# Optimization experiments

Hardware: AMD Instinct MI355X
Metric: run time of the kernel (lower is better)

The kernel has to match this reference:

```python
import math
import jax, jax.numpy as jnp
import numpy as np

B, T, DIM, H = 2, 2048, 2048, 16
D = DIM // H  # head_dim = 128


def setup_inputs() -> dict:
    key = jax.random.key(0)
    ks = jax.random.split(key, 6)
    s = 0.02
    x = jax.random.normal(ks[0], (B, T, DIM), dtype=jnp.float32)
    # causal mask: True = keep, False = masked (matches masked_fill(mask==0, -inf))
    attn_mask = jnp.tril(jnp.ones((T, T), dtype=bool))[None, None, :, :]
    Wq = jax.random.normal(ks[1], (DIM, DIM), dtype=jnp.float32) * s
    Wk = jax.random.normal(ks[2], (DIM, D), dtype=jnp.float32) * s
    Wv = jax.random.normal(ks[3], (DIM, D), dtype=jnp.float32) * s
    Wo = jax.random.normal(ks[4], (DIM, DIM), dtype=jnp.float32) * s
    return {
        "x": x, "attn_mask": attn_mask,
        "Wq": Wq, "bq": jnp.zeros((DIM,), jnp.float32),
        "Wk": Wk, "bk": jnp.zeros((D,), jnp.float32),
        "Wv": Wv, "bv": jnp.zeros((D,), jnp.float32),
        "Wo": Wo, "bo": jnp.zeros((DIM,), jnp.float32),
    }


def _rope_freqs(t_len, d):
    inv_freq = 1.0 / (10000.0 ** (jnp.arange(0, d, 2, dtype=jnp.float32) / d))
    f = jnp.arange(t_len, dtype=jnp.float32)[:, None] * inv_freq[None, :]  # [T, d/2]
    # duplicate to full head dim so cos/sin align with rotate_half's half split
    cos = jnp.concatenate([jnp.cos(f), jnp.cos(f)], axis=-1)[None, None]  # [1,1,T,d]
    sin = jnp.concatenate([jnp.sin(f), jnp.sin(f)], axis=-1)[None, None]
    return cos, sin


def _rotate_half(u):
    d2 = u.shape[-1] // 2
    return jnp.concatenate([-u[..., d2:], u[..., :d2]], axis=-1)


def reference(x, attn_mask, Wq, bq, Wk, bk, Wv, bv, Wo, bo):
    Bx, Tx, C = x.shape
    q = (x @ Wq + bq).reshape(Bx, Tx, H, D).transpose(0, 2, 1, 3)  # [B,H,T,D]
    k = (x @ Wk + bk)[:, None]  # [B,1,T,D] single shared KV head (MQA)
    v = (x @ Wv + bv)[:, None]
    cos, sin = _rope_freqs(Tx, D)
    q = q * cos + _rotate_half(q) * sin
    k = k * cos + _rotate_half(k) * sin
    attn = jnp.matmul(q, k.swapaxes(-2, -1)) / math.sqrt(D)  # [B,H,T,T]
    attn = jnp.where(attn_mask, attn, jnp.float32(-jnp.inf))
    attn = jax.nn.softmax(attn, axis=-1)
    out = jnp.matmul(attn, v)  # [B,H,T,D]
    out = out.transpose(0, 2, 1, 3).reshape(Bx, Tx, C)
    return out @ Wo + bo
```

## Files before the change

kernel.cpp:

```cpp
#include <hip/hip_runtime.h>

typedef unsigned short u16;
typedef unsigned int u32;
typedef __bf16 bf16x8 __attribute__((ext_vector_type(8)));
typedef float f32x4 __attribute__((ext_vector_type(4)));
typedef float f32x16 __attribute__((ext_vector_type(16)));
typedef u32 u32x4 __attribute__((ext_vector_type(4)));

__device__ __forceinline__ u16 bfu(float x) {
  union { __bf16 h; u16 u; } z; z.h = (__bf16)x; return z.u;
}
__device__ __forceinline__ u32 pk2(float a, float b) {
  union { __bf16 h[2]; u32 u; } z;
  z.h[0] = (__bf16)a; z.h[1] = (__bf16)b;
  return z.u;
}
__device__ __forceinline__ void gl_lds16(const u16* g, u16* l) {
  __builtin_amdgcn_global_load_lds((const __attribute__((address_space(1))) void*)g,
                                   (__attribute__((address_space(3))) void*)l, 16, 0, 0);
}

__global__ __launch_bounds__(256) void cvt_bf16(const float* __restrict__ src, u16* __restrict__ dst, int n8) {
  int i = blockIdx.x * 256 + threadIdx.x;
  if (i >= n8) return;
  const float4* s4 = (const float4*)src;
  float4 a = s4[2 * i], b = s4[2 * i + 1];
  u32x4 o;
  o[0] = pk2(a.x, a.y); o[1] = pk2(a.z, a.w);
  o[2] = pk2(b.x, b.y); o[3] = pk2(b.z, b.w);
  ((u32x4*)dst)[i] = o;
}

__global__ void transpose_cvt(const float* __restrict__ src, u16* __restrict__ dst, int R, int C) {
  __shared__ float tile[32][33];
  const int c0 = blockIdx.x * 32, r0 = blockIdx.y * 32;
  const int tx = threadIdx.x, ty = threadIdx.y;
#pragma unroll
  for (int i = 0; i < 4; ++i)
    tile[ty + i * 8][tx] = src[(size_t)(r0 + ty + i * 8) * C + c0 + tx];
  __syncthreads();
#pragma unroll
  for (int i = 0; i < 4; ++i)
    dst[(size_t)(c0 + ty + i * 8) * R + r0 + tx] = bfu(tile[tx][ty + i * 8]);
}

__global__ void transpose_v(const float* __restrict__ QKV, const float* __restrict__ bv, u16* __restrict__ Vt) {
  __shared__ float tile[32][33];
  const int t0 = blockIdx.x * 32, d0 = blockIdx.y * 32, b = blockIdx.z;
  const int tx = threadIdx.x, ty = threadIdx.y;
#pragma unroll
  for (int i = 0; i < 4; ++i)
    tile[ty + i * 8][tx] = QKV[(size_t)(b * 2048 + t0 + ty + i * 8) * 2304 + 2176 + d0 + tx] + bv[d0 + tx];
  __syncthreads();
#pragma unroll
  for (int i = 0; i < 4; ++i)
    Vt[(size_t)b * 262144 + (size_t)(d0 + ty + i * 8) * 2048 + t0 + tx] = bfu(tile[tx][ty + i * 8]);
}

__global__ __launch_bounds__(256) void rope_qk(const float* __restrict__ QKV, const float* __restrict__ bq,
                                               const float* __restrict__ bk,
                                               u16* __restrict__ Qb, u16* __restrict__ Kb) {
  const int row = blockIdx.x;
  const int b = row >> 11, t = row & 2047;
  const int tid = threadIdx.x;
  const float* qrow = QKV + (size_t)row * 2304;
  const float scale = 0.1275173862437171f;
  const float nl2 = -0.20762050593046f;
#pragma unroll
  for (int it = 0; it < 4; ++it) {
    int idx = tid + it * 256;
    int h = idx >> 6, j = idx & 63;
    float q0 = qrow[h * 128 + j] + bq[h * 128 + j];
    float q1 = qrow[h * 128 + j + 64] + bq[h * 128 + j + 64];
    float ang = (float)t * exp2f((float)j * nl2);
    float s, c;
    __sincosf(ang, &s, &c);
    size_t o = ((size_t)((b * 16 + h) * 2048 + t)) * 128 + j;
    Qb[o]      = bfu((q0 * c - q1 * s) * scale);
    Qb[o + 64] = bfu((q1 * c + q0 * s) * scale);
  }
  if (tid < 64) {
    int j = tid;
    float k0 = qrow[2048 + j] + bk[j];
    float k1 = qrow[2048 + j + 64] + bk[j + 64];
    float ang = (float)t * exp2f((float)j * nl2);
    float s, c;
    __sincosf(ang, &s, &c);
    size_t o = (size_t)row * 128 + j;
    Kb[o]      = bfu(k0 * c - k1 * s);
    Kb[o + 64] = bfu(k1 * c + k0 * s);
  }
}

template <bool BIAS, int NTL>
__global__ __launch_bounds__(256) void gemm_bt(const u16* __restrict__ A, const u16* __restrict__ Bt,
                                               const float* __restrict__ bias, float* __restrict__ C,
                                               int M, int N, int K) {
  const int lin = blockIdx.x;
  const int xcd = lin & 7, idx = lin >> 3;
  constexpr int HALF = NTL / 2;
  const int ly = idx / HALF, lx = idx - ly * HALF;
  const int my = (xcd >> 1) * 8 + ly;
  const int nx = (xcd & 1) * HALF + lx;
  const int n0 = nx * 128, m0 = my * 128;
  const int tid = threadIdx.x, lane = tid & 63;
  const int wid = tid >> 6, wr = wid >> 1, wc = wid & 1;
  __shared__ __align__(16) u16 As[128 * 32];
  __shared__ __align__(16) u16 Bs[128 * 32];
  f32x4 acc[4][4];
#pragma unroll
  for (int i = 0; i < 4; ++i)
#pragma unroll
    for (int j = 0; j < 4; ++j)
#pragma unroll
      for (int rr = 0; rr < 4; ++rr) acc[i][j][rr] = 0.f;

  const int c0 = tid, c1 = tid + 256;
  const int ar0 = c0 >> 2, ac0 = (c0 & 3) * 8;
  const int ar1 = c1 >> 2, ac1 = (c1 & 3) * 8;
  const int r = lane & 15, g = lane >> 4;

  for (int k0 = 0; k0 < K; k0 += 32) {
    gl_lds16(A + (size_t)(m0 + ar0) * K + k0 + ac0, As + c0 * 8);
    gl_lds16(A + (size_t)(m0 + ar1) * K + k0 + ac1, As + c1 * 8);
    gl_lds16(Bt + (size_t)(n0 + ar0) * K + k0 + ac0, Bs + c0 * 8);
    gl_lds16(Bt + (size_t)(n0 + ar1) * K + k0 + ac1, Bs + c1 * 8);
    __syncthreads();
    bf16x8 af[4], bfr[4];
#pragma unroll
    for (int mi = 0; mi < 4; ++mi)
      af[mi] = *reinterpret_cast<const bf16x8*>(&As[(wr * 64 + mi * 16 + r) * 32 + g * 8]);
#pragma unroll
    for (int ni = 0; ni < 4; ++ni)
      bfr[ni] = *reinterpret_cast<const bf16x8*>(&Bs[(wc * 64 + ni * 16 + r) * 32 + g * 8]);
#pragma unroll
    for (int mi = 0; mi < 4; ++mi)
#pragma unroll
      for (int ni = 0; ni < 4; ++ni)
        acc[mi][ni] = __builtin_amdgcn_mfma_f32_16x16x32_bf16(af[mi], bfr[ni], acc[mi][ni], 0, 0, 0);
    __syncthreads();
  }
#pragma unroll
  for (int mi = 0; mi < 4; ++mi)
#pragma unroll
    for (int ni = 0; ni < 4; ++ni) {
      int col = n0 + wc * 64 + ni * 16 + r;
      float bia = BIAS ? bias[col] : 0.f;
#pragma unroll
      for (int reg = 0; reg < 4; ++reg) {
        int row = m0 + wr * 64 + mi * 16 + g * 4 + reg;
        C[(size_t)row * N + col] = acc[mi][ni][reg] + bia;
      }
    }
}

__global__ __launch_bounds__(256, 2) void attn_kernel(const u16* __restrict__ Qb, const u16* __restrict__ Kb,
                                                      const u16* __restrict__ Vt, u16* __restrict__ Ob) {
  const int bid = blockIdx.x;
  const int grp = bid >> 5;
  const int chunk = (bid < 256) ? (15 - grp) : (grp - 8);
  const int bh = bid & 31, h = bh & 15, b = bh >> 4;
  const int tid = threadIdx.x, wid = tid >> 6, lane = tid & 63;
  const int l31 = lane & 31, hf = lane >> 5;

  __shared__ __align__(16) u16 smem[32768];
  u16* Ksb = smem;
  u16* Vsb = smem + 16384;

  const u16* Kbase = Kb + (size_t)b * 2048 * 128;
  const u16* Vbase = Vt + (size_t)b * 128 * 2048;

  int krow[4], kcol[4], vrow[4], vcol[4];
#pragma unroll
  for (int i = 0; i < 4; ++i) {
    const int seg = wid * 4 + i;
    const int r = seg * 4 + (lane >> 4);
    krow[i] = r; kcol[i] = (((lane & 15) ^ (r & 15)) << 3);
    const int d = seg * 8 + (lane >> 3);
    vrow[i] = d; vcol[i] = (((lane & 7) ^ (d & 7)) << 3);
  }
  const int ldsoff = wid * 2048 + lane * 8;

#define STAGE(buf, kvb_) do {                                                              \
    _Pragma("unroll") for (int i_ = 0; i_ < 4; ++i_)                                       \
      gl_lds16(Kbase + (size_t)((kvb_) + krow[i_]) * 128 + kcol[i_],                       \
               &Ksb[(buf) * 8192 + ldsoff + i_ * 512]);                                    \
    _Pragma("unroll") for (int i_ = 0; i_ < 4; ++i_)                                       \
      gl_lds16(Vbase + (size_t)vrow[i_] * 2048 + (kvb_) + vcol[i_],                        \
               &Vsb[(buf) * 8192 + ldsoff + i_ * 512]);                                    \
  } while (0)

  const int xk16 = l31 & 15;
  const int xk8 = l31 & 7;

  const int cb = chunk * 128;
  const int qw = cb + wid * 32;
  const u16* qptr = Qb + ((size_t)((b * 16 + h) * 2048 + qw + l31)) * 128;
  bf16x8 qf[8];
#pragma unroll
  for (int c = 0; c < 8; ++c)
    qf[c] = *reinterpret_cast<const bf16x8*>(qptr + c * 16 + hf * 8);

  f32x16 ot[4];
#pragma unroll
  for (int dt = 0; dt < 4; ++dt)
#pragma unroll
    for (int rr = 0; rr < 16; ++rr) ot[dt][rr] = 0.f;
  float m = -1e30f, lsum = 0.f;

  const int nkv = 2 * chunk + 2;
  STAGE(0, 0);
  for (int it = 0; it < nkv; ++it) {
    const int kvb = it << 6, cur = it & 1;
    if (it + 1 < nkv) {
      STAGE(cur ^ 1, kvb + 64);
      asm volatile("s_waitcnt vmcnt(8)" ::: "memory");
    } else {
      asm volatile("s_waitcnt vmcnt(0)" ::: "memory");
    }
    __builtin_amdgcn_s_barrier();

    if (kvb <= qw) {
      const u16* ks = Ksb + cur * 8192;
      const u16* vs = Vsb + cur * 8192;
      f32x16 st0, st1;
#pragma unroll
      for (int rr = 0; rr < 16; ++rr) { st0[rr] = 0.f; st1[rr] = -1e30f; }
      const u16* ksr0 = ks + l31 * 128;
#pragma unroll
      for (int c = 0; c < 8; ++c) {
        bf16x8 kf = *reinterpret_cast<const bf16x8*>(ksr0 + (((2 * c + hf) ^ xk16) << 3));
        st0 = __builtin_amdgcn_mfma_f32_32x32x16_bf16(kf, qf[c], st0, 0, 0, 0);
      }
      const bool a1 = (kvb + 32 <= qw);
      if (a1) {
#pragma unroll
        for (int rr = 0; rr < 16; ++rr) st1[rr] = 0.f;
        const u16* ksr1 = ks + (32 + l31) * 128;
#pragma unroll
        for (int c = 0; c < 8; ++c) {
          bf16x8 kf = *reinterpret_cast<const bf16x8*>(ksr1 + (((2 * c + hf) ^ xk16) << 3));
          st1 = __builtin_amdgcn_mfma_f32_32x32x16_bf16(kf, qf[c], st1, 0, 0, 0);
        }
        if (kvb + 32 == qw) {
#pragma unroll
          for (int rr = 0; rr < 16; ++rr) {
            int kvl = (rr & 3) + 8 * (rr >> 2) + 4 * hf;
            if (kvl > l31) st1[rr] = -1e30f;
          }
        }
      }
      if (kvb == qw) {
#pragma unroll
        for (int rr = 0; rr < 16; ++rr) {
          int kvl = (rr & 3) + 8 * (rr >> 2) + 4 * hf;
          if (kvl > l31) st0[rr] = -1e30f;
        }
      }

      float tmax = st0[0];
#pragma unroll
      for (int rr = 1; rr < 16; ++rr) tmax = fmaxf(tmax, st0[rr]);
#pragma unroll
      for (int rr = 0; rr < 16; ++rr) tmax = fmaxf(tmax, st1[rr]);
      tmax = fmaxf(tmax, __shfl_xor(tmax, 32, 64));
      if (!__all(tmax - m <= 8.f)) {
        const float mnew = fmaxf(m, tmax);
        const float alpha = exp2f(m - mnew);
        lsum *= alpha;
#pragma unroll
        for (int dt = 0; dt < 4; ++dt)
#pragma unroll
          for (int rr = 0; rr < 16; ++rr) ot[dt][rr] *= alpha;
        m = mnew;
      }
      float rsum = 0.f;
#pragma unroll
      for (int rr = 0; rr < 16; ++rr) { st0[rr] = exp2f(st0[rr] - m); rsum += st0[rr]; }
#pragma unroll
      for (int rr = 0; rr < 16; ++rr) { st1[rr] = exp2f(st1[rr] - m); rsum += st1[rr]; }
      rsum += __shfl_xor(rsum, 32, 64);
      lsum += rsum;

#pragma unroll
      for (int n = 0; n < 2; ++n) {
        if (n == 1 && !a1) break;
        const f32x16& pp = n ? st1 : st0;
#pragma unroll
        for (int s = 0; s < 2; ++s) {
          u32 a0p = pk2(pp[8 * s + 0], pp[8 * s + 1]);
          u32 a1p = pk2(pp[8 * s + 2], pp[8 * s + 3]);
          u32 b0p = pk2(pp[8 * s + 4], pp[8 * s + 5]);
          u32 b1p = pk2(pp[8 * s + 6], pp[8 * s + 7]);
          u32 k0 = hf ? b0p : a0p, k1 = hf ? b1p : a1p;
          u32 sd0 = hf ? a0p : b0p, sd1 = hf ? a1p : b1p;
          u32 r0 = (u32)__shfl_xor((int)sd0, 32, 64);
          u32 r1 = (u32)__shfl_xor((int)sd1, 32, 64);
          u32x4 pw;
          pw[0] = hf ? r0 : k0; pw[1] = hf ? r1 : k1;
          pw[2] = hf ? k0 : r0; pw[3] = hf ? k1 : r1;
          bf16x8 pb = __builtin_bit_cast(bf16x8, pw);
          const int cc = n * 4 + s * 2 + hf;
#pragma unroll
          for (int dt = 0; dt < 4; ++dt) {
            bf16x8 vf = *reinterpret_cast<const bf16x8*>(
                &vs[(dt * 32 + l31) * 64 + ((cc ^ xk8) << 3)]);
            ot[dt] = __builtin_amdgcn_mfma_f32_32x32x16_bf16(vf, pb, ot[dt], 0, 0, 0);
          }
        }
      }
    }
    __builtin_amdgcn_s_barrier();
  }

  u16* myt = smem + wid * (32 * 136);
  const float inv = 1.f / lsum;
#pragma unroll
  for (int dt = 0; dt < 4; ++dt)
#pragma unroll
    for (int rq = 0; rq < 4; ++rq) {
      int d = dt * 32 + 8 * rq + 4 * hf;
      u32 lo = pk2(ot[dt][rq * 4 + 0] * inv, ot[dt][rq * 4 + 1] * inv);
      u32 hi = pk2(ot[dt][rq * 4 + 2] * inv, ot[dt][rq * 4 + 3] * inv);
      u32* dstp = (u32*)&myt[l31 * 136 + d];
      dstp[0] = lo; dstp[1] = hi;
    }
  __syncthreads();
  const size_t outbase = ((size_t)(b * 2048 + qw)) * 2048 + h * 128;
#pragma unroll
  for (int i = 0; i < 8; ++i) {
    int chunk2 = i * 64 + lane;
    int row = chunk2 >> 4, c16 = chunk2 & 15;
    u32x4 v = *reinterpret_cast<const u32x4*>(&myt[row * 136 + c16 * 8]);
    *reinterpret_cast<u32x4*>(Ob + outbase + (size_t)row * 2048 + c16 * 8) = v;
  }
#undef STAGE
}

extern "C" void kernel_launch(void* const* d_in, const int* in_sizes, int n_in,
                              void* d_out, int out_size, void* d_ws, size_t ws_size,
                              hipStream_t stream) {
  const float* x  = (const float*)d_in[0];
  const float* Wq = (const float*)d_in[2];
  const float* bq = (const float*)d_in[3];
  const float* Wk = (const float*)d_in[4];
  const float* bk = (const float*)d_in[5];
  const float* Wv = (const float*)d_in[6];
  const float* bv = (const float*)d_in[7];
  const float* Wo = (const float*)d_in[8];
  const float* bo = (const float*)d_in[9];

  char* ws = (char*)d_ws;
  u16*  xb    = (u16*)ws;   ws += (size_t)4096 * 2048 * 2;
  u16*  WqkvT = (u16*)ws;   ws += (size_t)2304 * 2048 * 2;
  u16*  WoT   = (u16*)ws;   ws += (size_t)2048 * 2048 * 2;
  float* QKV  = (float*)ws; ws += (size_t)4096 * 2304 * 4;
  u16*  Qb    = (u16*)ws;   ws += (size_t)2 * 16 * 2048 * 128 * 2;
  u16*  Kb    = (u16*)ws;   ws += (size_t)2 * 2048 * 128 * 2;
  u16*  Vt    = (u16*)ws;   ws += (size_t)2 * 128 * 2048 * 2;
  u16*  Ob    = (u16*)ws;   ws += (size_t)4096 * 2048 * 2;

  dim3 tb(32, 8);
  cvt_bf16<<<4096, 256, 0, stream>>>(x, xb, 1048576);
  transpose_cvt<<<dim3(64, 64), tb, 0, stream>>>(Wq, WqkvT, 2048, 2048);
  transpose_cvt<<<dim3(4, 64),  tb, 0, stream>>>(Wk, WqkvT + (size_t)2048 * 2048, 2048, 128);
  transpose_cvt<<<dim3(4, 64),  tb, 0, stream>>>(Wv, WqkvT + (size_t)2176 * 2048, 2048, 128);
  transpose_cvt<<<dim3(64, 64), tb, 0, stream>>>(Wo, WoT, 2048, 2048);

  gemm_bt<false, 18><<<576, 256, 0, stream>>>(xb, WqkvT, nullptr, QKV, 4096, 2304, 2048);
  rope_qk<<<4096, 256, 0, stream>>>(QKV, bq, bk, Qb, Kb);
  transpose_v<<<dim3(64, 4, 2), tb, 0, stream>>>(QKV, bv, Vt);
  attn_kernel<<<512, 256, 0, stream>>>(Qb, Kb, Vt, Ob);
  gemm_bt<true, 16><<<512, 256, 0, stream>>>(Ob, WoT, bo, (float*)d_out, 4096, 2048, 2048);
}
```

Before: 223.9 us.

## Split long causal query chunks across two KV partitions with a combine kernel

The eight longest query chunks (c=8..15) are split into two blocks, each covering half of the KV range, which raises the attention grid from 512 to 768 blocks and evens out per-block work. Partial outputs in fp32 plus the running max and sum are written to workspace, and a new combine kernel merges them with a log-sum-exp rescale and writes bf16. This targets load imbalance and tail effects from the causal triangle. The cost is an extra kernel launch and extra fp32 global traffic.

New measurement: 240.4 us. +7.3%, slower.

```diff
diff --git a/kernel.cpp b/kernel.cpp
--- a/kernel.cpp
+++ b/kernel.cpp
@@ -155,11 +155,17 @@
 }
 
 __global__ __launch_bounds__(256, 2) void attn_kernel(const u16* __restrict__ Qb, const u16* __restrict__ Kb,
-                                                      const u16* __restrict__ Vt, u16* __restrict__ Ob) {
-  const int bid = blockIdx.x;
-  const int grp = bid >> 5;
-  const int chunk = (bid < 256) ? (15 - grp) : (grp - 8);
-  const int bh = bid & 31, h = bh & 15, b = bh >> 4;
+                                                      const u16* __restrict__ Vt, u16* __restrict__ Ob,
+                                                      float* __restrict__ Opart, float2* __restrict__ Ostat) {
+  const int pid = blockIdx.x;
+  const int local = pid >> 5, bh = pid & 31;
+  const int h = bh & 15, b = bh >> 4;
+  int c, part, npart;
+  if (local < 16) { c = 15 - (local >> 1); part = local & 1; npart = 2; }
+  else            { c = 23 - local;        part = 0;         npart = 1; }
+  const int tlo = part * (c + 1);
+  const int thi = (npart == 2 && part == 0) ? (c + 1) : (2 * c + 2);
+
   const int tid = threadIdx.x, wid = tid >> 6, lane = tid & 63;
   const int l31 = lane & 31, hf = lane >> 5;
 
@@ -193,13 +199,12 @@
   const int xk16 = l31 & 15;
   const int xk8 = l31 & 7;
 
-  const int cb = chunk * 128;
-  const int qw = cb + wid * 32;
+  const int qw = c * 128 + wid * 32;
   const u16* qptr = Qb + ((size_t)((b * 16 + h) * 2048 + qw + l31)) * 128;
   bf16x8 qf[8];
 #pragma unroll
-  for (int c = 0; c < 8; ++c)
-    qf[c] = *reinterpret_cast<const bf16x8*>(qptr + c * 16 + hf * 8);
+  for (int cc2 = 0; cc2 < 8; ++cc2)
+    qf[cc2] = *reinterpret_cast<const bf16x8*>(qptr + cc2 * 16 + hf * 8);
 
   f32x16 ot[4];
 #pragma unroll
@@ -208,11 +213,10 @@
     for (int rr = 0; rr < 16; ++rr) ot[dt][rr] = 0.f;
   float m = -1e30f, lsum = 0.f;
 
-  const int nkv = 2 * chunk + 2;
-  STAGE(0, 0);
-  for (int it = 0; it < nkv; ++it) {
-    const int kvb = it << 6, cur = it & 1;
-    if (it + 1 < nkv) {
+  STAGE(0, tlo * 64);
+  for (int it = tlo; it < thi; ++it) {
+    const int kvb = it << 6, cur = (it - tlo) & 1;
+    if (it + 1 < thi) {
       STAGE(cur ^ 1, kvb + 64);
       asm volatile("s_waitcnt vmcnt(8)" ::: "memory");
     } else {
@@ -228,9 +232,9 @@
       for (int rr = 0; rr < 16; ++rr) { st0[rr] = 0.f; st1[rr] = -1e30f; }
       const u16* ksr0 = ks + l31 * 128;
 #pragma unroll
-      for (int c = 0; c < 8; ++c) {
-        bf16x8 kf = *reinterpret_cast<const bf16x8*>(ksr0 + (((2 * c + hf) ^ xk16) << 3));
-        st0 = __builtin_amdgcn_mfma_f32_32x32x16_bf16(kf, qf[c], st0, 0, 0, 0);
+      for (int cc2 = 0; cc2 < 8; ++cc2) {
+        bf16x8 kf = *reinterpret_cast<const bf16x8*>(ksr0 + (((2 * cc2 + hf) ^ xk16) << 3));
+        st0 = __builtin_amdgcn_mfma_f32_32x32x16_bf16(kf, qf[cc2], st0, 0, 0, 0);
       }
       const bool a1 = (kvb + 32 <= qw);
       if (a1) {
@@ -238,9 +242,9 @@
         for (int rr = 0; rr < 16; ++rr) st1[rr] = 0.f;
         const u16* ksr1 = ks + (32 + l31) * 128;
 #pragma unroll
-        for (int c = 0; c < 8; ++c) {
-          bf16x8 kf = *reinterpret_cast<const bf16x8*>(ksr1 + (((2 * c + hf) ^ xk16) << 3));
-          st1 = __builtin_amdgcn_mfma_f32_32x32x16_bf16(kf, qf[c], st1, 0, 0, 0);
+        for (int cc2 = 0; cc2 < 8; ++cc2) {
+          bf16x8 kf = *reinterpret_cast<const bf16x8*>(ksr1 + (((2 * cc2 + hf) ^ xk16) << 3));
+          st1 = __builtin_amdgcn_mfma_f32_32x32x16_bf16(kf, qf[cc2], st1, 0, 0, 0);
         }
         if (kvb + 32 == qw) {
 #pragma unroll
@@ -313,28 +317,78 @@
     __builtin_amdgcn_s_barrier();
   }
 
-  u16* myt = smem + wid * (32 * 136);
-  const float inv = 1.f / lsum;
-#pragma unroll
-  for (int dt = 0; dt < 4; ++dt)
-#pragma unroll
-    for (int rq = 0; rq < 4; ++rq) {
-      int d = dt * 32 + 8 * rq + 4 * hf;
-      u32 lo = pk2(ot[dt][rq * 4 + 0] * inv, ot[dt][rq * 4 + 1] * inv);
-      u32 hi = pk2(ot[dt][rq * 4 + 2] * inv, ot[dt][rq * 4 + 3] * inv);
-      u32* dstp = (u32*)&myt[l31 * 136 + d];
-      dstp[0] = lo; dstp[1] = hi;
+  if (npart == 1) {
+    u16* myt = smem + wid * (32 * 136);
+    const float inv = 1.f / lsum;
+#pragma unroll
+    for (int dt = 0; dt < 4; ++dt)
+#pragma unroll
+      for (int rq = 0; rq < 4; ++rq) {
+        int d = dt * 32 + 8 * rq + 4 * hf;
+        u32 lo = pk2(ot[dt][rq * 4 + 0] * inv, ot[dt][rq * 4 + 1] * inv);
+        u32 hi = pk2(ot[dt][rq * 4 + 2] * inv, ot[dt][rq * 4 + 3] * inv);
+        u32* dstp = (u32*)&myt[l31 * 136 + d];
+        dstp[0] = lo; dstp[1] = hi;
+      }
+    __syncthreads();
+    const size_t outbase = ((size_t)(b * 2048 + qw)) * 2048 + h * 128;
+#pragma unroll
+    for (int i = 0; i < 8; ++i) {
+      int chunk2 = i * 64 + lane;
+      int row = chunk2 >> 4, c16 = chunk2 & 15;
+      u32x4 v = *reinterpret_cast<const u32x4*>(&myt[row * 136 + c16 * 8]);
+      *reinterpret_cast<u32x4*>(Ob + outbase + (size_t)row * 2048 + c16 * 8) = v;
     }
-  __syncthreads();
-  const size_t outbase = ((size_t)(b * 2048 + qw)) * 2048 + h * 128;
+  } else {
+    const int pslot = (((c - 8) << 5) + bh) * 2 + part;
+    if (hf == 0) {
+      float2 st; st.x = m; st.y = lsum;
+      Ostat[pslot * 128 + wid * 32 + l31] = st;
+    }
+    float* Op = Opart + (size_t)pslot * 16384 + (size_t)(wid * 32 + l31) * 128;
+#pragma unroll
+    for (int dt = 0; dt < 4; ++dt)
+#pragma unroll
+      for (int rq = 0; rq < 4; ++rq) {
+        f32x4 v;
+        v[0] = ot[dt][rq * 4 + 0]; v[1] = ot[dt][rq * 4 + 1];
+        v[2] = ot[dt][rq * 4 + 2]; v[3] = ot[dt][rq * 4 + 3];
+        *reinterpret_cast<f32x4*>(Op + dt * 32 + 8 * rq + 4 * hf) = v;
+      }
+  }
+#undef STAGE
+}
+
+__global__ __launch_bounds__(256) void attn_combine(const float* __restrict__ Opart,
+                                                    const float2* __restrict__ Ostat,
+                                                    u16* __restrict__ Ob) {
+  const int gid = blockIdx.x;
+  const int cm = gid >> 5, bh = gid & 31;
+  const int c = cm + 8, h = bh & 15, b = bh >> 4;
+  const int tid = threadIdx.x;
+  const int row = tid >> 1, half = tid & 1;
+  const int p0 = gid * 2, p1 = p0 + 1;
+  const float2 s0 = Ostat[p0 * 128 + row];
+  const float2 s1 = Ostat[p1 * 128 + row];
+  const float M = fmaxf(s0.x, s1.x);
+  float a0 = exp2f(s0.x - M), a1 = exp2f(s1.x - M);
+  const float inv = 1.f / (a0 * s0.y + a1 * s1.y);
+  a0 *= inv; a1 *= inv;
+  const f32x4* O0 = (const f32x4*)(Opart + (size_t)p0 * 16384 + row * 128 + half * 64);
+  const f32x4* O1 = (const f32x4*)(Opart + (size_t)p1 * 16384 + row * 128 + half * 64);
+  u32 w[32];
+#pragma unroll
+  for (int i = 0; i < 16; ++i) {
+    f32x4 v0 = O0[i], v1 = O1[i];
+    w[i * 2]     = pk2(a0 * v0[0] + a1 * v1[0], a0 * v0[1] + a1 * v1[1]);
+    w[i * 2 + 1] = pk2(a0 * v0[2] + a1 * v1[2], a0 * v0[3] + a1 * v1[3]);
+  }
+  u16* dst = Ob + ((size_t)(b * 2048 + c * 128 + row)) * 2048 + h * 128 + half * 64;
 #pragma unroll
   for (int i = 0; i < 8; ++i) {
-    int chunk2 = i * 64 + lane;
-    int row = chunk2 >> 4, c16 = chunk2 & 15;
-    u32x4 v = *reinterpret_cast<const u32x4*>(&myt[row * 136 + c16 * 8]);
-    *reinterpret_cast<u32x4*>(Ob + outbase + (size_t)row * 2048 + c16 * 8) = v;
-  }
-#undef STAGE
+    u32x4 v; v[0] = w[i * 4]; v[1] = w[i * 4 + 1]; v[2] = w[i * 4 + 2]; v[3] = w[i * 4 + 3];
+    ((u32x4*)dst)[i] = v;
+  }
 }
 
 extern "C" void kernel_launch(void* const* d_in, const int* in_sizes, int n_in,
@@ -359,6 +413,8 @@
   u16*  Kb    = (u16*)ws;   ws += (size_t)2 * 2048 * 128 * 2;
   u16*  Vt    = (u16*)ws;   ws += (size_t)2 * 128 * 2048 * 2;
   u16*  Ob    = (u16*)ws;   ws += (size_t)4096 * 2048 * 2;
+  float* Opart = (float*)ws; ws += (size_t)512 * 128 * 128 * 4;
+  float2* Ostat = (float2*)ws; ws += (size_t)512 * 128 * 8;
 
   dim3 tb(32, 8);
   cvt_bf16<<<4096, 256, 0, stream>>>(x, xb, 1048576);
@@ -370,6 +426,7 @@
   gemm_bt<false, 18><<<576, 256, 0, stream>>>(xb, WqkvT, nullptr, QKV, 4096, 2304, 2048);
   rope_qk<<<4096, 256, 0, stream>>>(QKV, bq, bk, Qb, Kb);
   transpose_v<<<dim3(64, 4, 2), tb, 0, stream>>>(QKV, bv, Vt);
-  attn_kernel<<<512, 256, 0, stream>>>(Qb, Kb, Vt, Ob);
+  attn_kernel<<<768, 256, 0, stream>>>(Qb, Kb, Vt, Ob, Opart, Ostat);
+  attn_combine<<<256, 256, 0, stream>>>(Opart, Ostat, Ob);
   gemm_bt<true, 16><<<512, 256, 0, stream>>>(Ob, WoT, bo, (float*)d_out, 4096, 2048, 2048);
 }
```

## Split attention into 64-row, 2-wave blocks with single-buffered KV and MFMA priority

Applied to the files above, without the earlier changes.

Attention blocks shrink from 4 waves covering 128 query rows to 2 waves covering 64 rows. The grid doubles to 1024 blocks, ordered longest-chunk first, which should give finer causal load balance and let more blocks share a CU. KV staging changes from double-buffered prefetch to a single buffer that is loaded and then synchronised, halving LDS per block but exposing load latency inside each iteration. s_setprio raises wave priority around the MFMA sections, and the per-wave causal skip of whole tiles is dropped because every wave now needs each staged tile.

Measured after the change: 236.9 us. 1.06x slower.

```diff
diff --git a/kernel.cpp b/kernel.cpp
--- a/kernel.cpp
+++ b/kernel.cpp
@@ -154,47 +154,45 @@
     }
 }
 
-__global__ __launch_bounds__(256, 2) void attn_kernel(const u16* __restrict__ Qb, const u16* __restrict__ Kb,
+__global__ __launch_bounds__(128, 2) void attn_kernel(const u16* __restrict__ Qb, const u16* __restrict__ Kb,
                                                       const u16* __restrict__ Vt, u16* __restrict__ Ob) {
   const int bid = blockIdx.x;
-  const int grp = bid >> 5;
-  const int chunk = (bid < 256) ? (15 - grp) : (grp - 8);
+  const int chunk = 31 - (bid >> 5);
   const int bh = bid & 31, h = bh & 15, b = bh >> 4;
   const int tid = threadIdx.x, wid = tid >> 6, lane = tid & 63;
   const int l31 = lane & 31, hf = lane >> 5;
 
-  __shared__ __align__(16) u16 smem[32768];
-  u16* Ksb = smem;
-  u16* Vsb = smem + 16384;
+  __shared__ __align__(16) u16 smem[16384];
+  u16* Ks = smem;
+  u16* Vs = smem + 8192;
 
   const u16* Kbase = Kb + (size_t)b * 2048 * 128;
   const u16* Vbase = Vt + (size_t)b * 128 * 2048;
 
-  int krow[4], kcol[4], vrow[4], vcol[4];
-#pragma unroll
-  for (int i = 0; i < 4; ++i) {
-    const int seg = wid * 4 + i;
+  int krow[8], kcol[8], vrow[8], vcol[8];
+#pragma unroll
+  for (int i = 0; i < 8; ++i) {
+    const int seg = wid * 8 + i;
     const int r = seg * 4 + (lane >> 4);
     krow[i] = r; kcol[i] = (((lane & 15) ^ (r & 15)) << 3);
     const int d = seg * 8 + (lane >> 3);
     vrow[i] = d; vcol[i] = (((lane & 7) ^ (d & 7)) << 3);
   }
-  const int ldsoff = wid * 2048 + lane * 8;
-
-#define STAGE(buf, kvb_) do {                                                              \
-    _Pragma("unroll") for (int i_ = 0; i_ < 4; ++i_)                                       \
+  const int ldsoff = wid * 4096 + lane * 8;
+
+#define STAGE(kvb_) do {                                                                   \
+    _Pragma("unroll") for (int i_ = 0; i_ < 8; ++i_)                                       \
       gl_lds16(Kbase + (size_t)((kvb_) + krow[i_]) * 128 + kcol[i_],                       \
-               &Ksb[(buf) * 8192 + ldsoff + i_ * 512]);                                    \
-    _Pragma("unroll") for (int i_ = 0; i_ < 4; ++i_)                                       \
+               &Ks[ldsoff + i_ * 512]);                                                    \
+    _Pragma("unroll") for (int i_ = 0; i_ < 8; ++i_)                                       \
       gl_lds16(Vbase + (size_t)vrow[i_] * 2048 + (kvb_) + vcol[i_],                        \
-               &Vsb[(buf) * 8192 + ldsoff + i_ * 512]);                                    \
+               &Vs[ldsoff + i_ * 512]);                                                    \
   } while (0)
 
   const int xk16 = l31 & 15;
   const int xk8 = l31 & 7;
 
-  const int cb = chunk * 128;
-  const int qw = cb + wid * 32;
+  const int qw = chunk * 64 + wid * 32;
   const u16* qptr = Qb + ((size_t)((b * 16 + h) * 2048 + qw + l31)) * 128;
   bf16x8 qf[8];
 #pragma unroll
@@ -208,109 +206,105 @@
     for (int rr = 0; rr < 16; ++rr) ot[dt][rr] = 0.f;
   float m = -1e30f, lsum = 0.f;
 
-  const int nkv = 2 * chunk + 2;
-  STAGE(0, 0);
+  const int nkv = chunk + 1;
   for (int it = 0; it < nkv; ++it) {
-    const int kvb = it << 6, cur = it & 1;
-    if (it + 1 < nkv) {
-      STAGE(cur ^ 1, kvb + 64);
-      asm volatile("s_waitcnt vmcnt(8)" ::: "memory");
-    } else {
-      asm volatile("s_waitcnt vmcnt(0)" ::: "memory");
-    }
-    __builtin_amdgcn_s_barrier();
-
-    if (kvb <= qw) {
-      const u16* ks = Ksb + cur * 8192;
-      const u16* vs = Vsb + cur * 8192;
-      f32x16 st0, st1;
-#pragma unroll
-      for (int rr = 0; rr < 16; ++rr) { st0[rr] = 0.f; st1[rr] = -1e30f; }
-      const u16* ksr0 = ks + l31 * 128;
+    const int kvb = it << 6;
+    STAGE(kvb);
+    __syncthreads();
+
+    f32x16 st0, st1;
+#pragma unroll
+    for (int rr = 0; rr < 16; ++rr) { st0[rr] = 0.f; st1[rr] = -1e30f; }
+    const u16* ksr0 = Ks + l31 * 128;
+    __builtin_amdgcn_s_setprio(1);
+#pragma unroll
+    for (int c = 0; c < 8; ++c) {
+      bf16x8 kf = *reinterpret_cast<const bf16x8*>(ksr0 + (((2 * c + hf) ^ xk16) << 3));
+      st0 = __builtin_amdgcn_mfma_f32_32x32x16_bf16(kf, qf[c], st0, 0, 0, 0);
+    }
+    __builtin_amdgcn_s_setprio(0);
+    const bool a1 = (kvb + 32 <= qw);
+    if (a1) {
+#pragma unroll
+      for (int rr = 0; rr < 16; ++rr) st1[rr] = 0.f;
+      const u16* ksr1 = Ks + (32 + l31) * 128;
+      __builtin_amdgcn_s_setprio(1);
 #pragma unroll
       for (int c = 0; c < 8; ++c) {
-        bf16x8 kf = *reinterpret_cast<const bf16x8*>(ksr0 + (((2 * c + hf) ^ xk16) << 3));
-        st0 = __builtin_amdgcn_mfma_f32_32x32x16_bf16(kf, qf[c], st0, 0, 0, 0);
-      }
-      const bool a1 = (kvb + 32 <= qw);
-      if (a1) {
-#pragma unroll
-        for (int rr = 0; rr < 16; ++rr) st1[rr] = 0.f;
-        const u16* ksr1 = ks + (32 + l31) * 128;
-#pragma unroll
-        for (int c = 0; c < 8; ++c) {
-          bf16x8 kf = *reinterpret_cast<const bf16x8*>(ksr1 + (((2 * c + hf) ^ xk16) << 3));
-          st1 = __builtin_amdgcn_mfma_f32_32x32x16_bf16(kf, qf[c], st1, 0, 0, 0);
-        }
-        if (kvb + 32 == qw) {
-#pragma unroll
-          for (int rr = 0; rr < 16; ++rr) {
-            int kvl = (rr & 3) + 8 * (rr >> 2) + 4 * hf;
-            if (kvl > l31) st1[rr] = -1e30f;
-          }
-        }
-      }
-      if (kvb == qw) {
+        bf16x8 kf = *reinterpret_cast<const bf16x8*>(ksr1 + (((2 * c + hf) ^ xk16) << 3));
+        st1 = __builtin_amdgcn_mfma_f32_32x32x16_bf16(kf, qf[c], st1, 0, 0, 0);
+      }
+      __builtin_amdgcn_s_setprio(0);
+      if (kvb + 32 == qw) {
 #pragma unroll
         for (int rr = 0; rr < 16; ++rr) {
           int kvl = (rr & 3) + 8 * (rr >> 2) + 4 * hf;
-          if (kvl > l31) st0[rr] = -1e30f;
+          if (kvl > l31) st1[rr] = -1e30f;
         }
       }
-
-      float tmax = st0[0];
-#pragma unroll
-      for (int rr = 1; rr < 16; ++rr) tmax = fmaxf(tmax, st0[rr]);
-#pragma unroll
-      for (int rr = 0; rr < 16; ++rr) tmax = fmaxf(tmax, st1[rr]);
-      tmax = fmaxf(tmax, __shfl_xor(tmax, 32, 64));
-      if (!__all(tmax - m <= 8.f)) {
-        const float mnew = fmaxf(m, tmax);
-        const float alpha = exp2f(m - mnew);
-        lsum *= alpha;
-#pragma unroll
-        for (int dt = 0; dt < 4; ++dt)
-#pragma unroll
-          for (int rr = 0; rr < 16; ++rr) ot[dt][rr] *= alpha;
-        m = mnew;
-      }
-      float rsum = 0.f;
-#pragma unroll
-      for (int rr = 0; rr < 16; ++rr) { st0[rr] = exp2f(st0[rr] - m); rsum += st0[rr]; }
-#pragma unroll
-      for (int rr = 0; rr < 16; ++rr) { st1[rr] = exp2f(st1[rr] - m); rsum += st1[rr]; }
-      rsum += __shfl_xor(rsum, 32, 64);
-      lsum += rsum;
-
-#pragma unroll
-      for (int n = 0; n < 2; ++n) {
-        if (n == 1 && !a1) break;
-        const f32x16& pp = n ? st1 : st0;
-#pragma unroll
-        for (int s = 0; s < 2; ++s) {
-          u32 a0p = pk2(pp[8 * s + 0], pp[8 * s + 1]);
-          u32 a1p = pk2(pp[8 * s + 2], pp[8 * s + 3]);
-          u32 b0p = pk2(pp[8 * s + 4], pp[8 * s + 5]);
-          u32 b1p = pk2(pp[8 * s + 6], pp[8 * s + 7]);
-          u32 k0 = hf ? b0p : a0p, k1 = hf ? b1p : a1p;
-          u32 sd0 = hf ? a0p : b0p, sd1 = hf ? a1p : b1p;
-          u32 r0 = (u32)__shfl_xor((int)sd0, 32, 64);
-          u32 r1 = (u32)__shfl_xor((int)sd1, 32, 64);
-          u32x4 pw;
-          pw[0] = hf ? r0 : k0; pw[1] = hf ? r1 : k1;
-          pw[2] = hf ? k0 : r0; pw[3] = hf ? k1 : r1;
-          bf16x8 pb = __builtin_bit_cast(bf16x8, pw);
-          const int cc = n * 4 + s * 2 + hf;
-#pragma unroll
-          for (int dt = 0; dt < 4; ++dt) {
-            bf16x8 vf = *reinterpret_cast<const bf16x8*>(
-                &vs[(dt * 32 + l31) * 64 + ((cc ^ xk8) << 3)]);
-            ot[dt] = __builtin_amdgcn_mfma_f32_32x32x16_bf16(vf, pb, ot[dt], 0, 0, 0);
-          }
+    }
+    if (kvb == qw) {
+#pragma unroll
+      for (int rr = 0; rr < 16; ++rr) {
+        int kvl = (rr & 3) + 8 * (rr >> 2) + 4 * hf;
+        if (kvl > l31) st0[rr] = -1e30f;
+      }
+    }
+
+    float tmax = st0[0];
+#pragma unroll
+    for (int rr = 1; rr < 16; ++rr) tmax = fmaxf(tmax, st0[rr]);
+#pragma unroll
+    for (int rr = 0; rr < 16; ++rr) tmax = fmaxf(tmax, st1[rr]);
+    tmax = fmaxf(tmax, __shfl_xor(tmax, 32, 64));
+    if (!__all(tmax - m <= 8.f)) {
+      const float mnew = fmaxf(m, tmax);
+      const float alpha = exp2f(m - mnew);
+      lsum *= alpha;
+#pragma unroll
+      for (int dt = 0; dt < 4; ++dt)
+#pragma unroll
+        for (int rr = 0; rr < 16; ++rr) ot[dt][rr] *= alpha;
+      m = mnew;
+    }
+    float rsum = 0.f;
+#pragma unroll
+    for (int rr = 0; rr < 16; ++rr) { st0[rr] = exp2f(st0[rr] - m); rsum += st0[rr]; }
+#pragma unroll
+    for (int rr = 0; rr < 16; ++rr) { st1[rr] = exp2f(st1[rr] - m); rsum += st1[rr]; }
+    rsum += __shfl_xor(rsum, 32, 64);
+    lsum += rsum;
+
+#pragma unroll
+    for (int n = 0; n < 2; ++n) {
+      if (n == 1 && !a1) break;
+      const f32x16& pp = n ? st1 : st0;
+#pragma unroll
+      for (int s = 0; s < 2; ++s) {
+        u32 a0p = pk2(pp[8 * s + 0], pp[8 * s + 1]);
+        u32 a1p = pk2(pp[8 * s + 2], pp[8 * s + 3]);
+        u32 b0p = pk2(pp[8 * s + 4], pp[8 * s + 5]);
+        u32 b1p = pk2(pp[8 * s + 6], pp[8 * s + 7]);
+        u32 k0 = hf ? b0p : a0p, k1 = hf ? b1p : a1p;
+        u32 sd0 = hf ? a0p : b0p, sd1 = hf ? a1p : b1p;
+        u32 r0 = (u32)__shfl_xor((int)sd0, 32, 64);
+        u32 r1 = (u32)__shfl_xor((int)sd1, 32, 64);
+        u32x4 pw;
+        pw[0] = hf ? r0 : k0; pw[1] = hf ? r1 : k1;
+        pw[2] = hf ? k0 : r0; pw[3] = hf ? k1 : r1;
+        bf16x8 pb = __builtin_bit_cast(bf16x8, pw);
+        const int cc = n * 4 + s * 2 + hf;
+        __builtin_amdgcn_s_setprio(1);
+#pragma unroll
+        for (int dt = 0; dt < 4; ++dt) {
+          bf16x8 vf = *reinterpret_cast<const bf16x8*>(
+              &Vs[(dt * 32 + l31) * 64 + ((cc ^ xk8) << 3)]);
+          ot[dt] = __builtin_amdgcn_mfma_f32_32x32x16_bf16(vf, pb, ot[dt], 0, 0, 0);
         }
-      }
-    }
-    __builtin_amdgcn_s_barrier();
+        __builtin_amdgcn_s_setprio(0);
+      }
+    }
+    __syncthreads();
   }
 
   u16* myt = smem + wid * (32 * 136);
@@ -370,6 +364,6 @@
   gemm_bt<false, 18><<<576, 256, 0, stream>>>(xb, WqkvT, nullptr, QKV, 4096, 2304, 2048);
   rope_qk<<<4096, 256, 0, stream>>>(QKV, bq, bk, Qb, Kb);
   transpose_v<<<dim3(64, 4, 2), tb, 0, stream>>>(QKV, bv, Vt);
-  attn_kernel<<<512, 256, 0, stream>>>(Qb, Kb, Vt, Ob);
+  attn_kernel<<<1024, 128, 0, stream>>>(Qb, Kb, Vt, Ob);
   gemm_bt<true, 16><<<512, 256, 0, stream>>>(Ob, WoT, bo, (float*)d_out, 4096, 2048, 2048);
 }
```
